# Performance work log

Measured on AMD Instinct MI355X. Metric: run time of the kernel, lower is better.

## Reference

```python
import jax, jax.numpy as jnp
import numpy as np
from jax import lax

N_G, E_G, E_LG = 100000, 400000, 1200000
N_T, E_T, E_LGT = 50000, 100000, 300000
D_F, D_MSG_G = 64, 128
VOCAB, D_EMB, D_MSG_T = 780, 128, 128
N_ITERS_G, N_ITERS_T = 4, 4
SCALE = 0.05  # keep relu/sum chains numerically tame over iterations


def setup_inputs() -> dict:
    key = jax.random.key(0)
    ks = jax.random.split(key, 32)
    f32 = jnp.float32
    w = lambda k, sh: jax.random.normal(k, sh, f32) * SCALE
    return {
        "G_f": jax.random.normal(ks[0], (N_G, D_F), f32),
        "G_ef": jax.random.normal(ks[1], (E_G, D_F), f32),
        "G_src": jax.random.randint(ks[2], (E_G,), 0, N_G, jnp.int32),
        "G_dst": jax.random.randint(ks[3], (E_G,), 0, N_G, jnp.int32),
        "G_lg_src": jax.random.randint(ks[4], (E_LG,), 0, E_G, jnp.int32),
        "G_lg_dst": jax.random.randint(ks[5], (E_LG,), 0, E_G, jnp.int32),
        "T_id": jax.random.randint(ks[6], (N_T,), 0, VOCAB, jnp.int32),
        "T_src": jax.random.randint(ks[7], (E_T,), 0, N_T, jnp.int32),
        "T_dst": jax.random.randint(ks[8], (E_T,), 0, N_T, jnp.int32),
        "T_lg_src": jax.random.randint(ks[9], (E_LGT,), 0, E_T, jnp.int32),
        "T_lg_dst": jax.random.randint(ks[10], (E_LGT,), 0, E_T, jnp.int32),
        "embeddings": jax.random.normal(ks[11], (VOCAB, D_EMB), f32),
        "W1": w(ks[12], (D_F, D_MSG_G)),
        "W2": w(ks[13], (D_F, D_MSG_G)),
        "W3": w(ks[14], (D_MSG_G, D_MSG_G)),
        "U1_G": w(ks[15], (D_F, D_MSG_G)),
        "U2_G": w(ks[16], (D_MSG_G, D_MSG_G)),
        "Wz": w(ks[17], (D_EMB, D_MSG_T)),
        "Uz": w(ks[18], (D_MSG_T, D_MSG_T)),
        "Wr": w(ks[19], (D_EMB, D_MSG_T)),
        "Ur": w(ks[20], (D_MSG_T, D_MSG_T)),
        "Wh": w(ks[21], (D_EMB, D_MSG_T)),
        "Uh": w(ks[22], (D_MSG_T, D_MSG_T)),
        "U1_T": w(ks[23], (D_EMB, D_MSG_T)),
        "U2_T": w(ks[24], (D_MSG_T, D_MSG_T)),
    }


def reference(G_f, G_ef, G_src, G_dst, G_lg_src, G_lg_dst,
              T_id, T_src, T_dst, T_lg_src, T_lg_dst,
              embeddings, W1, W2, W3, U1_G, U2_G,
              Wz, Uz, Wr, Ur, Wh, Uh, U1_T, U2_T):
    seg = jax.ops.segment_sum

    # ---- molecule graph G: loopy-BP MLP messages on the line graph ----
    f_src_G = G_f[G_src]                               # [E_G, D_F] copy_src
    base_G = f_src_G @ W1 + G_ef @ W2                  # loop-invariant part of g1_G

    def stepG(msg, _):
        sum_msg = seg(msg[G_lg_src], G_lg_dst, num_segments=E_G)
        return jax.nn.relu(base_G + sum_msg @ W3), None

    msgG0 = jnp.zeros((E_G, D_MSG_G), G_f.dtype)
    msgG, _ = lax.scan(stepG, msgG0, None, length=N_ITERS_G)

    # readout g2_G: sum edge msgs into dst nodes
    sG = seg(msgG, G_dst, num_segments=N_G)
    x_G = jax.nn.relu(G_f @ U1_G + sG @ U2_G)          # [N_G, D_MSG_G]

    # ---- junction tree T: GRU messages on the tree line graph ----
    f_T = embeddings[T_id]                             # one-hot id @ embeddings
    f_src_T = f_T[T_src]                               # [E_T, D_EMB]
    xz, xr, xh = f_src_T @ Wz, f_src_T @ Wr, f_src_T @ Wh

    def stepT(msg, _):
        s = seg(msg[T_lg_src], T_lg_dst, num_segments=E_T)
        z = jax.nn.sigmoid(xz + s @ Uz)
        r = jax.nn.sigmoid(xr + s @ Ur)
        h = jnp.tanh(xh + (r * s) @ Uh)
        return (1.0 - z) * s + z * h, None

    msgT0 = jnp.zeros((E_T, D_MSG_T), f_T.dtype)
    msgT, _ = lax.scan(stepT, msgT0, None, length=N_ITERS_T)

    sT = seg(msgT, T_dst, num_segments=N_T)
    x_T = jax.nn.relu(f_T @ U1_T + sT @ U2_T)          # [N_T, D_MSG_T]

    # concat node readouts (same width) so output is a single array
    return jnp.concatenate([x_G, x_T], axis=0)         # [N_G+N_T, 128]
```

## Files before the change

### kernel.cpp

```cpp
#include <hip/hip_runtime.h>

#define NG 100000
#define EG 400000
#define ELG 1200000
#define NT 50000
#define ET 100000
#define ELGT 300000

#define GEG ((EG + 63) / 64)
#define GET ((ET + 63) / 64)
#define GNG ((NG + 63) / 64)
#define GNT ((NT + 63) / 64)

#define SEG1 EG
#define SEG2 (EG + NG)
#define SEG3 (EG + NG + ET)
#define NSEG_ALL (EG + NG + ET + NT)
#define NE_ALL (ELG + EG + ELGT + ET)
#define NE_PAD (NE_ALL + 3 * NSEG_ALL + 64)

typedef unsigned short u16;
typedef unsigned int u32;
typedef __attribute__((ext_vector_type(8))) short bf16x8;
typedef __attribute__((ext_vector_type(4))) float f32x4;

#define TILE_B 16384

__device__ __forceinline__ float bflo(u32 p){ return __uint_as_float(p << 16); }
__device__ __forceinline__ float bfhi(u32 p){ return __uint_as_float(p & 0xffff0000u); }
__device__ __forceinline__ float bf2f(u16 h){ return __uint_as_float(((u32)h) << 16); }
__device__ __forceinline__ u16 f2bf(float f){
  u32 u = __float_as_uint(f);
  u32 r = u + 0x7fffu + ((u >> 16) & 1u);
  return (u16)(r >> 16);
}
__device__ __forceinline__ float sigm(float x){ return 1.0f / (1.0f + __expf(-x)); }
__device__ __forceinline__ float tanh_(float x){ return 2.0f / (1.0f + __expf(-2.0f * x)) - 1.0f; }
__device__ __forceinline__ float relu_(float x){ return x > 0.0f ? x : 0.0f; }
__device__ __forceinline__ void wfence(){ __builtin_amdgcn_wave_barrier(); }

__device__ __forceinline__ int swz(int r, int c){ return r * 256 + (c ^ ((r & 7) << 4)); }

__device__ __forceinline__ void zero8(float v[8]){
  #pragma unroll
  for (int j = 0; j < 8; j++) v[j] = 0.f;
}
__device__ __forceinline__ uint4 pack8(const float v[8]){
  uint4 o;
  o.x = f2bf(v[0]) | ((u32)f2bf(v[1]) << 16);
  o.y = f2bf(v[2]) | ((u32)f2bf(v[3]) << 16);
  o.z = f2bf(v[4]) | ((u32)f2bf(v[5]) << 16);
  o.w = f2bf(v[6]) | ((u32)f2bf(v[7]) << 16);
  return o;
}
__device__ __forceinline__ uint2 pack4(const f32x4& a){
  uint2 o;
  o.x = (u32)f2bf(a[0]) | ((u32)f2bf(a[1]) << 16);
  o.y = (u32)f2bf(a[2]) | ((u32)f2bf(a[3]) << 16);
  return o;
}
__device__ __forceinline__ void unp4(uint2 u, float v[4]){
  v[0] = bflo(u.x); v[1] = bfhi(u.x); v[2] = bflo(u.y); v[3] = bfhi(u.y);
}
__device__ __forceinline__ bf16x8 packfrag(const float v[8]){
  union { uint4 u; bf16x8 b; } c; c.u = pack8(v); return c.b;
}
__device__ __forceinline__ bf16x8 zfrag(){
  union { uint4 u; bf16x8 b; } c; c.u = make_uint4(0, 0, 0, 0); return c.b;
}
__device__ __forceinline__ bf16x8 as_frag(uint4 u){
  union { uint4 u; bf16x8 b; } c; c.u = u; return c.b;
}

__global__ void k_sniff(const u32* __restrict__ g, int* __restrict__ flag){
  __shared__ int sh[2];
  if (threadIdx.x < 2) sh[threadIdx.x] = 0;
  __syncthreads();
  int c0 = 0, c1 = 0;
  for (int i = 0; i < 16; i++){
    u32 w = g[threadIdx.x * 16 + i];
    u32 lo = w & 0xFFFFu;
    if (lo == 0u) c0++;
    else { u32 e = (lo >> 7) & 0xFFu; if (e >= 96u && e <= 144u) c1++; }
  }
  atomicAdd(&sh[0], c0); atomicAdd(&sh[1], c1);
  __syncthreads();
  if (threadIdx.x == 0) *flag = (sh[0] < 512 && sh[1] > 2048) ? 1 : 0;
}

__global__ void k_cvt_all(const void* p0, const void* p1, const void* p2, const void* p3,
                          const void* p4, const void* p5, const void* p6, const void* p7,
                          const void* p8, const void* p9, const void* p10, const void* p11,
                          const void* p12, float* __restrict__ wm, const int* __restrict__ flagp){
  int i = blockIdx.x * 256 + threadIdx.x;
  if (i >= 188416) return;
  const int offs[14] = {0,8192,16384,32768,40960,57344,73728,90112,106496,122880,139264,155648,172032,188416};
  const void* ps[13] = {p0,p1,p2,p3,p4,p5,p6,p7,p8,p9,p10,p11,p12};
  int w = 0;
  while (i >= offs[w + 1]) w++;
  int li = i - offs[w];
  wm[i] = (*flagp) ? bf2f(((const u16*)ps[w])[li]) : ((const float*)ps[w])[li];
}

__global__ void k_mkfrag_all(const float* __restrict__ wm, u16* __restrict__ frag){
  const int wmo[13] = {0,8192,16384,32768,40960,57344,73728,90112,106496,122880,139264,155648,172032};
  const int nks[13] = {2,2,4,2,4,4,4,4,4,4,4,4,4};
  int b = blockIdx.x;
  int wi = 0, ks = b;
  while (ks >= nks[wi]){ ks -= nks[wi]; wi++; }
  const float* W = wm + wmo[wi];
  int nt = threadIdx.x >> 6, lane = threadIdx.x & 63;
  int kr = ks * 32 + ((lane >> 4) << 3);
  int col = nt * 16 + (lane & 15);
  u16* o = frag + (size_t)b * 4096 + nt * 512 + lane * 8;
  #pragma unroll
  for (int j = 0; j < 8; j++) o[j] = f2bf(W[(size_t)(kr + j) * 128 + col]);
}

__device__ __forceinline__ const void* rowdt(const void* mat, size_t row, int W, int bf){
  return bf ? (const void*)((const u16*)mat + row * (size_t)W)
            : (const void*)((const float*)mat + row * (size_t)W);
}
__device__ __forceinline__ void load8(const void* rowbase, int c8, int bf, float v[8]){
  if (bf){
    uint4 d = ((const uint4*)rowbase)[c8];
    v[0]=bflo(d.x); v[1]=bfhi(d.x); v[2]=bflo(d.y); v[3]=bfhi(d.y);
    v[4]=bflo(d.z); v[5]=bfhi(d.z); v[6]=bflo(d.w); v[7]=bfhi(d.w);
  } else {
    const float4* p = (const float4*)rowbase + (c8 << 1);
    float4 a = p[0], b = p[1];
    v[0]=a.x; v[1]=a.y; v[2]=a.z; v[3]=a.w; v[4]=b.x; v[5]=b.y; v[6]=b.z; v[7]=b.w;
  }
}

__global__ void k_hist_all(const int* __restrict__ Glgd, const int* __restrict__ Gd,
                           const int* __restrict__ Tlgd, const int* __restrict__ Td,
                           int* __restrict__ cnt){
  int e = blockIdx.x * 256 + threadIdx.x;
  if (e >= NE_ALL) return;
  int seg;
  if (e < ELG)                       seg = Glgd[e];
  else if (e < ELG + EG)             seg = SEG1 + Gd[e - ELG];
  else if (e < ELG + EG + ELGT)      seg = SEG2 + Tlgd[e - ELG - EG];
  else                               seg = SEG3 + Td[e - ELG - EG - ELGT];
  atomicAdd(&cnt[seg], 1);
}

__global__ void k_scan1(const int* __restrict__ cnt, int n, int* __restrict__ csum){
  int base = blockIdx.x * 4096, tid = threadIdx.x;
  int s = 0;
  for (int i = 0; i < 16; i++){
    int idx = base + i * 256 + tid;
    if (idx < n) s += (cnt[idx] + 3) & ~3;
  }
  __shared__ int red[4];
  for (int off = 32; off; off >>= 1) s += __shfl_down(s, off, 64);
  if ((tid & 63) == 0) red[tid >> 6] = s;
  __syncthreads();
  if (tid == 0) csum[blockIdx.x] = red[0] + red[1] + red[2] + red[3];
}

__global__ void k_scan2(int* csum, int nch, int* rowptr, int n){
  if (threadIdx.x == 0){
    int run = 0;
    for (int c = 0; c < nch; c++){ int t = csum[c]; csum[c] = run; run += t; }
    rowptr[n] = run;
  }
}

__global__ void k_scan3(const int* __restrict__ cnt, int n, const int* __restrict__ csum,
                        int* __restrict__ rowptr){
  __shared__ int buf[4096];
  __shared__ int tsum[256];
  int base = blockIdx.x * 4096, tid = threadIdx.x;
  for (int i = 0; i < 16; i++){
    int idx = base + i * 256 + tid;
    buf[i * 256 + tid] = (idx < n) ? ((cnt[idx] + 3) & ~3) : 0;
  }
  __syncthreads();
  int run = 0;
  for (int i = 0; i < 16; i++){ int v = buf[tid * 16 + i]; buf[tid * 16 + i] = run; run += v; }
  tsum[tid] = run;
  __syncthreads();
  for (int off = 1; off < 256; off <<= 1){
    int v = (tid >= off) ? tsum[tid - off] : 0;
    __syncthreads();
    tsum[tid] += v;
    __syncthreads();
  }
  int texcl = tsum[tid] - run;
  int cbase = csum[blockIdx.x];
  for (int i = 0; i < 16; i++){
    int idx = base + tid * 16 + i;
    if (idx < n) rowptr[idx] = cbase + texcl + buf[tid * 16 + i];
  }
}

__global__ void k_fill_all(const int* __restrict__ Glgd, const int* __restrict__ Glgs,
                           const int* __restrict__ Gd,
                           const int* __restrict__ Tlgd, const int* __restrict__ Tlgs,
                           const int* __restrict__ Td,
                           const int* __restrict__ rowptr, int* __restrict__ fill,
                           int* __restrict__ col){
  int e = blockIdx.x * 256 + threadIdx.x;
  if (e >= NE_ALL) return;
  int seg, srcv;
  if (e < ELG){                      seg = Glgd[e];                           srcv = Glgs[e]; }
  else if (e < ELG + EG){            int l = e - ELG;                         seg = SEG1 + Gd[l];   srcv = l; }
  else if (e < ELG + EG + ELGT){     int l = e - ELG - EG;                    seg = SEG2 + Tlgd[l]; srcv = Tlgs[l]; }
  else {                             int l = e - ELG - EG - ELGT;             seg = SEG3 + Td[l];   srcv = l; }
  int pos = atomicAdd(&fill[seg], 1);
  col[rowptr[seg] + pos] = srcv;
}

__global__ void k_fill_pad(const int* __restrict__ cnt, const int* __restrict__ rowptr,
                           int* __restrict__ col){
  int seg = blockIdx.x * 256 + threadIdx.x;
  if (seg >= NSEG_ALL) return;
  int dummy = (seg < SEG2) ? EG : ET;
  int start = rowptr[seg] + cnt[seg];
  int end = rowptr[seg + 1];
  for (int q = start; q < end; q++) col[q] = dummy;
}

__global__ void k_zero_dummy(u16* a, u16* b, u16* c, u16* d){
  int i = threadIdx.x;
  if (i < 128){
    a[(size_t)EG * 128 + i] = 0; b[(size_t)EG * 128 + i] = 0;
    c[(size_t)ET * 128 + i] = 0; d[(size_t)ET * 128 + i] = 0;
  }
}


__device__ __forceinline__ void acc8_add(float (&a)[8], uint4 d){
  a[0] += bflo(d.x); a[1] += bfhi(d.x);
  a[2] += bflo(d.y); a[3] += bfhi(d.y);
  a[4] += bflo(d.z); a[5] += bfhi(d.z);
  a[6] += bflo(d.w); a[7] += bfhi(d.w);
}

__device__ __forceinline__ void gather_accum(const int* __restrict__ rowptr,
    const int* __restrict__ colidx, const u16* __restrict__ msg,
    int row, int M, int kg, float (&acc)[4][8])
{
  #pragma unroll
  for (int ks = 0; ks < 4; ks++) zero8(acc[ks]);
  if (row >= M) return;
  int p = rowptr[row], pe = rowptr[row + 1];
  for (; p < pe; p += 4){
    int i0 = colidx[p], i1 = colidx[p + 1], i2 = colidx[p + 2], i3 = colidx[p + 3];
    const uint4* b0 = (const uint4*)(msg + (size_t)i0 * 128);
    const uint4* b1 = (const uint4*)(msg + (size_t)i1 * 128);
    const uint4* b2 = (const uint4*)(msg + (size_t)i2 * 128);
    const uint4* b3 = (const uint4*)(msg + (size_t)i3 * 128);
    uint4 v0[4], v1[4], v2[4], v3[4];
    #pragma unroll
    for (int ks = 0; ks < 4; ks++){
      v0[ks] = b0[ks * 4 + kg]; v1[ks] = b1[ks * 4 + kg];
      v2[ks] = b2[ks * 4 + kg]; v3[ks] = b3[ks * 4 + kg];
    }
    #pragma unroll
    for (int ks = 0; ks < 4; ks++){
      acc8_add(acc[ks], v0[ks]); acc8_add(acc[ks], v1[ks]);
      acc8_add(acc[ks], v2[ks]); acc8_add(acc[ks], v3[ks]);
    }
  }
}

template<int KS>
__device__ __forceinline__ void mma_f(const bf16x8* a, const u16* __restrict__ frag,
                                      f32x4 (&acc)[8])
{
  int lane = threadIdx.x & 63;
  #pragma unroll
  for (int ks = 0; ks < KS; ks++){
    const u16* fb = frag + (size_t)ks * 4096 + lane * 8;
    #pragma unroll
    for (int nt = 0; nt < 8; nt++){
      bf16x8 b = *(const bf16x8*)(fb + (size_t)nt * 512);
      acc[nt] = __builtin_amdgcn_mfma_f32_16x16x32_bf16(a[ks], b, acc[nt], 0, 0, 0);
    }
  }
}

#define INIT_ACC(A) { _Pragma("unroll") for (int n_=0;n_<8;n_++){ A[n_][0]=0.f; A[n_][1]=0.f; A[n_][2]=0.f; A[n_][3]=0.f; } }

__device__ __forceinline__ void repack_store(const char* __restrict__ tile,
    u16* __restrict__ dst, int row0, int M)
{
  int rl = threadIdx.x >> 2, q = threadIdx.x & 3;
  int grow = row0 + rl;
  if (grow < M){
    #pragma unroll
    for (int v = 0; v < 4; v++){
      uint4 d = *(const uint4*)(tile + swz(rl, (v * 4 + q) * 16));
      *(uint4*)(dst + (size_t)grow * 128 + (size_t)(v * 4 + q) * 8) = d;
    }
  }
}

__device__ __forceinline__ size_t fslot(int blk, int w, int nt){
  return ((((size_t)blk * 4 + w) * 8 + nt) * 64 + (threadIdx.x & 63)) * 4;
}

__device__ __forceinline__ void load_catfrag(const void* __restrict__ Gf,
    const void* __restrict__ Gef, const int* __restrict__ Gsrc,
    int arow, int kg, int bf, bf16x8 (&fC)[4])
{
  if (arow < EG){
    int sr = Gsrc[arow];
    const void* ra = rowdt(Gf, (size_t)sr, 64, bf);
    const void* rb = rowdt(Gef, (size_t)arow, 64, bf);
    float t[8];
    load8(ra, kg, bf, t);     fC[0] = packfrag(t);
    load8(ra, 4 + kg, bf, t); fC[1] = packfrag(t);
    load8(rb, kg, bf, t);     fC[2] = packfrag(t);
    load8(rb, 4 + kg, bf, t); fC[3] = packfrag(t);
  } else {
    #pragma unroll
    for (int ks = 0; ks < 4; ks++) fC[ks] = zfrag();
  }
}


__global__ __launch_bounds__(256, 4) void k_init(
    const void* __restrict__ Gf, const void* __restrict__ Gef, const int* __restrict__ Gsrc,
    const u16* __restrict__ fWcat, const int* __restrict__ flagp, u16* __restrict__ msgG,
    const void* __restrict__ emb, const int* __restrict__ Tid, const int* __restrict__ Tsrc,
    const u16* __restrict__ fWz, const u16* __restrict__ fWr, const u16* __restrict__ fWh,
    u16* __restrict__ xzf, u16* __restrict__ xrf, u16* __restrict__ xhf, u16* __restrict__ msgT)
{
  __shared__ char t0[TILE_B];
  int bf = *flagp;
  int lane = threadIdx.x & 63, w = threadIdx.x >> 6;
  int stripe = w * 16, kg = lane >> 4, m16 = lane & 15;
  if (blockIdx.x < GET){
    int blk = blockIdx.x, row0 = blk * 64, arow = row0 + stripe + m16;
    bf16x8 fE[4];
    if (arow < ET){
      int id = Tid[Tsrc[arow]];
      const void* rb = rowdt(emb, (size_t)id, 128, bf);
      #pragma unroll
      for (int ks = 0; ks < 4; ks++){
        float t[8]; load8(rb, ks * 4 + kg, bf, t); fE[ks] = packfrag(t);
      }
    } else {
      #pragma unroll
      for (int ks = 0; ks < 4; ks++) fE[ks] = zfrag();
    }
    f32x4 acc[8];
    uint2 zpk[8];
    INIT_ACC(acc);
    mma_f<4>(fE, fWz, acc);
    #pragma unroll
    for (int nt = 0; nt < 8; nt++){
      zpk[nt] = pack4(acc[nt]);
      *(uint2*)(xzf + fslot(blk, w, nt)) = zpk[nt];
    }
    INIT_ACC(acc);
    mma_f<4>(fE, fWr, acc);
    #pragma unroll
    for (int nt = 0; nt < 8; nt++)
      *(uint2*)(xrf + fslot(blk, w, nt)) = pack4(acc[nt]);
    INIT_ACC(acc);
    mma_f<4>(fE, fWh, acc);
    #pragma unroll
    for (int nt = 0; nt < 8; nt++){
      *(uint2*)(xhf + fslot(blk, w, nt)) = pack4(acc[nt]);
      float xzv[4]; unp4(zpk[nt], xzv);
      #pragma unroll
      for (int r = 0; r < 4; r++){
        int rt = stripe + (kg << 2) + r;
        int cb = nt * 32 + m16 * 2;
        *(u16*)(t0 + swz(rt, cb)) = f2bf(sigm(xzv[r]) * tanh_(acc[nt][r]));
      }
    }
    wfence();
    repack_store(t0, msgT, row0, ET);
  } else {
    int blk = blockIdx.x - GET, row0 = blk * 64, arow = row0 + stripe + m16;
    bf16x8 fC[4];
    load_catfrag(Gf, Gef, Gsrc, arow, kg, bf, fC);
    f32x4 acc[8]; INIT_ACC(acc);
    mma_f<4>(fC, fWcat, acc);
    #pragma unroll
    for (int nt = 0; nt < 8; nt++)
      #pragma unroll
      for (int r = 0; r < 4; r++){
        int rt = stripe + (kg << 2) + r;
        int cb = nt * 32 + m16 * 2;
        *(u16*)(t0 + swz(rt, cb)) = f2bf(relu_(acc[nt][r]));
      }
    wfence();
    repack_store(t0, msgG, row0, EG);
  }
}

__global__ __launch_bounds__(256, 4) void k_iter(
    const u16* __restrict__ msgInG, u16* __restrict__ msgOutG,
    const void* __restrict__ Gf, const void* __restrict__ Gef, const int* __restrict__ Gsrc,
    const int* __restrict__ rp, const int* __restrict__ col,
    const u16* __restrict__ fWcat, const u16* __restrict__ fW3, const int* __restrict__ flagp,
    const u16* __restrict__ msgInT, u16* __restrict__ msgOutT,
    const u16* __restrict__ fUz, const u16* __restrict__ fUr, const u16* __restrict__ fUh,
    const u16* __restrict__ xzf, const u16* __restrict__ xrf, const u16* __restrict__ xhf)
{
  __shared__ char t0[TILE_B];
  __shared__ char t1[TILE_B];
  int lane = threadIdx.x & 63, w = threadIdx.x >> 6;
  int stripe = w * 16, kg = lane >> 4, m16 = lane & 15;
  if (blockIdx.x < GET){
    int blk = blockIdx.x, row0 = blk * 64, arow = row0 + stripe + m16;
    float ga[4][8];
    gather_accum(rp + SEG2, col, msgInT, arow, ET, kg, ga);
    bf16x8 fS[4];
    #pragma unroll
    for (int ks = 0; ks < 4; ks++){
      uint4 pk = pack8(ga[ks]);
      *(uint4*)(t0 + swz(stripe + m16, ks * 64 + kg * 16)) = pk;
      fS[ks] = as_frag(pk);
    }
    f32x4 acc[8];
    INIT_ACC(acc);
    mma_f<4>(fS, fUr, acc);
    wfence();
    #pragma unroll
    for (int nt = 0; nt < 8; nt++){
      uint2 r4 = *(const uint2*)(xrf + fslot(blk, w, nt));
      float xrv[4]; unp4(r4, xrv);
      #pragma unroll
      for (int r = 0; r < 4; r++){
        int rt = stripe + (kg << 2) + r;
        int cb = nt * 32 + m16 * 2;
        float s = bf2f(*(const u16*)(t0 + swz(rt, cb)));
        float rr = sigm(xrv[r] + acc[nt][r]);
        *(u16*)(t1 + swz(rt, cb)) = f2bf(rr * s);
      }
    }
    wfence();
    bf16x8 fRS[4];
    #pragma unroll
    for (int ks = 0; ks < 4; ks++)
      fRS[ks] = *(const bf16x8*)(t1 + swz(stripe + m16, ks * 64 + kg * 16));
    INIT_ACC(acc);
    mma_f<4>(fRS, fUh, acc);
    wfence();
    #pragma unroll
    for (int nt = 0; nt < 8; nt++){
      uint2 h4 = *(const uint2*)(xhf + fslot(blk, w, nt));
      float xhv[4]; unp4(h4, xhv);
      #pragma unroll
      for (int r = 0; r < 4; r++){
        int rt = stripe + (kg << 2) + r;
        int cb = nt * 32 + m16 * 2;
        *(u16*)(t1 + swz(rt, cb)) = f2bf(tanh_(xhv[r] + acc[nt][r]));
      }
    }
    wfence();
    bf16x8 fS2[4];
    #pragma unroll
    for (int ks = 0; ks < 4; ks++)
      fS2[ks] = *(const bf16x8*)(t0 + swz(stripe + m16, ks * 64 + kg * 16));
    INIT_ACC(acc);
    mma_f<4>(fS2, fUz, acc);
    wfence();
    #pragma unroll
    for (int nt = 0; nt < 8; nt++){
      uint2 z4 = *(const uint2*)(xzf + fslot(blk, w, nt));
      float xzv[4]; unp4(z4, xzv);
      #pragma unroll
      for (int r = 0; r < 4; r++){
        int rt = stripe + (kg << 2) + r;
        int cb = nt * 32 + m16 * 2;
        float z = sigm(xzv[r] + acc[nt][r]);
        float s = bf2f(*(const u16*)(t0 + swz(rt, cb)));
        float h = bf2f(*(const u16*)(t1 + swz(rt, cb)));
        *(u16*)(t0 + swz(rt, cb)) = f2bf((1.f - z) * s + z * h);
      }
    }
    wfence();
    repack_store(t0, msgOutT, row0, ET);
  } else {
    int bf = *flagp;
    int blk = blockIdx.x - GET, row0 = blk * 64, arow = row0 + stripe + m16;
    float ga[4][8];
    gather_accum(rp, col, msgInG, arow, EG, kg, ga);
    bf16x8 fS[4];
    #pragma unroll
    for (int ks = 0; ks < 4; ks++) fS[ks] = packfrag(ga[ks]);
    bf16x8 fC[4];
    load_catfrag(Gf, Gef, Gsrc, arow, kg, bf, fC);
    f32x4 acc[8]; INIT_ACC(acc);
    mma_f<4>(fS, fW3, acc);
    mma_f<4>(fC, fWcat, acc);
    #pragma unroll
    for (int nt = 0; nt < 8; nt++)
      #pragma unroll
      for (int r = 0; r < 4; r++){
        int rt = stripe + (kg << 2) + r;
        int cb = nt * 32 + m16 * 2;
        *(u16*)(t0 + swz(rt, cb)) = f2bf(relu_(acc[nt][r]));
      }
    wfence();
    repack_store(t0, msgOutG, row0, EG);
  }
}

__global__ __launch_bounds__(256, 4) void k_readout(
    const void* __restrict__ Gf, const u16* __restrict__ msgG,
    const int* __restrict__ rp, const int* __restrict__ col,
    const u16* __restrict__ fU1G, const u16* __restrict__ fU2G,
    const void* __restrict__ emb, const int* __restrict__ Tid, const u16* __restrict__ msgT,
    const u16* __restrict__ fU1T, const u16* __restrict__ fU2T,
    const int* __restrict__ flagp, float* __restrict__ out)
{
  int bf = *flagp;
  int lane = threadIdx.x & 63, w = threadIdx.x >> 6;
  int stripe = w * 16, kg = lane >> 4, m16 = lane & 15;
  if (blockIdx.x < GNT){
    int row0 = blockIdx.x * 64, arow = row0 + stripe + m16;
    float ga[4][8];
    gather_accum(rp + SEG3, col, msgT, arow, NT, kg, ga);
    bf16x8 fS[4];
    #pragma unroll
    for (int ks = 0; ks < 4; ks++) fS[ks] = packfrag(ga[ks]);
    bf16x8 fE[4];
    if (arow < NT){
      int id = Tid[arow];
      const void* rb = rowdt(emb, (size_t)id, 128, bf);
      #pragma unroll
      for (int ks = 0; ks < 4; ks++){
        float t[8]; load8(rb, ks * 4 + kg, bf, t); fE[ks] = packfrag(t);
      }
    } else {
      #pragma unroll
      for (int ks = 0; ks < 4; ks++) fE[ks] = zfrag();
    }
    f32x4 acc[8]; INIT_ACC(acc);
    mma_f<4>(fS, fU2T, acc);
    mma_f<4>(fE, fU1T, acc);
    #pragma unroll
    for (int nt = 0; nt < 8; nt++)
      #pragma unroll
      for (int r = 0; r < 4; r++){
        int R = row0 + stripe + (kg << 2) + r;
        if (R < NT) out[(size_t)(NG + R) * 128 + nt * 16 + m16] = relu_(acc[nt][r]);
      }
  } else {
    int row0 = (blockIdx.x - GNT) * 64, arow = row0 + stripe + m16;
    float ga[4][8];
    gather_accum(rp + SEG1, col, msgG, arow, NG, kg, ga);
    bf16x8 fS[4];
    #pragma unroll
    for (int ks = 0; ks < 4; ks++) fS[ks] = packfrag(ga[ks]);
    bf16x8 fG[2];
    if (arow < NG){
      const void* ra = rowdt(Gf, (size_t)arow, 64, bf);
      float t[8];
      load8(ra, kg, bf, t);     fG[0] = packfrag(t);
      load8(ra, 4 + kg, bf, t); fG[1] = packfrag(t);
    } else { fG[0] = zfrag(); fG[1] = zfrag(); }
    f32x4 acc[8]; INIT_ACC(acc);
    mma_f<4>(fS, fU2G, acc);
    mma_f<2>(fG, fU1G, acc);
    #pragma unroll
    for (int nt = 0; nt < 8; nt++)
      #pragma unroll
      for (int r = 0; r < 4; r++){
        int R = row0 + stripe + (kg << 2) + r;
        if (R < NG) out[(size_t)R * 128 + nt * 16 + m16] = relu_(acc[nt][r]);
      }
  }
}

extern "C" void kernel_launch(void* const* d_in, const int* in_sizes, int n_in,
                              void* d_out, int out_size, void* d_ws, size_t ws_size,
                              hipStream_t stream)
{
  const void* G_f      = d_in[0];
  const void* G_ef     = d_in[1];
  const int*  G_src    = (const int*)d_in[2];
  const int*  G_dst    = (const int*)d_in[3];
  const int*  G_lg_src = (const int*)d_in[4];
  const int*  G_lg_dst = (const int*)d_in[5];
  const int*  T_id     = (const int*)d_in[6];
  const int*  T_src    = (const int*)d_in[7];
  const int*  T_dst    = (const int*)d_in[8];
  const int*  T_lg_src = (const int*)d_in[9];
  const int*  T_lg_dst = (const int*)d_in[10];
  const void* emb      = d_in[11];
  float* out = (float*)d_out;
  (void)in_sizes; (void)n_in; (void)out_size; (void)ws_size;

  size_t off = 0;
  auto alloc = [&](size_t bytes) -> char* {
    char* p = (char*)d_ws + off;
    off += (bytes + 255) & ~(size_t)255;
    return p;
  };

  int*   flag = (int*)alloc(256);
  float* wm   = (float*)alloc(sizeof(float) * 188416);
  u16*   frag = (u16*)alloc(2 * 46 * 4096);
  const u16* fWcat = frag;
  const u16* fW3   = frag + (size_t)4  * 4096;
  const u16* fU1G  = frag + (size_t)8  * 4096;
  const u16* fU2G  = frag + (size_t)10 * 4096;
  const u16* fWz   = frag + (size_t)14 * 4096;
  const u16* fUz   = frag + (size_t)18 * 4096;
  const u16* fWr   = frag + (size_t)22 * 4096;
  const u16* fUr   = frag + (size_t)26 * 4096;
  const u16* fWh   = frag + (size_t)30 * 4096;
  const u16* fUh   = frag + (size_t)34 * 4096;
  const u16* fU1T  = frag + (size_t)38 * 4096;
  const u16* fU2T  = frag + (size_t)42 * 4096;

  int* rp   = (int*)alloc(sizeof(int) * (NSEG_ALL + 1));
  int* col  = (int*)alloc(sizeof(int) * NE_PAD);
  int* cnt  = (int*)alloc(sizeof(int) * 2 * NSEG_ALL);
  int* csum = (int*)alloc(sizeof(int) * 256);
  u16* msgGA = (u16*)alloc((size_t)(EG + 1) * 128 * 2);
  u16* msgGB = (u16*)alloc((size_t)(EG + 1) * 128 * 2);
  u16* xzf   = (u16*)alloc((size_t)GET * 8192 * 2);
  u16* xrf   = (u16*)alloc((size_t)GET * 8192 * 2);
  u16* xhf   = (u16*)alloc((size_t)GET * 8192 * 2);
  u16* msgTA = (u16*)alloc((size_t)(ET + 1) * 128 * 2);
  u16* msgTB = (u16*)alloc((size_t)(ET + 1) * 128 * 2);

  k_sniff<<<1, 256, 0, stream>>>((const u32*)G_ef, flag);
  k_cvt_all<<<(188416 + 255) / 256, 256, 0, stream>>>(
      d_in[12], d_in[13], d_in[14], d_in[15], d_in[16], d_in[17], d_in[18],
      d_in[19], d_in[20], d_in[21], d_in[22], d_in[23], d_in[24], wm, flag);
  k_mkfrag_all<<<46, 512, 0, stream>>>(wm, frag);
  k_zero_dummy<<<1, 128, 0, stream>>>(msgGA, msgGB, msgTA, msgTB);

  hipMemsetAsync(cnt, 0, sizeof(int) * 2 * NSEG_ALL, stream);
  k_hist_all<<<(NE_ALL + 255) / 256, 256, 0, stream>>>(G_lg_dst, G_dst, T_lg_dst, T_dst, cnt);
  int nch = (NSEG_ALL + 4095) / 4096;
  k_scan1<<<nch, 256, 0, stream>>>(cnt, NSEG_ALL, csum);
  k_scan2<<<1, 64, 0, stream>>>(csum, nch, rp, NSEG_ALL);
  k_scan3<<<nch, 256, 0, stream>>>(cnt, NSEG_ALL, csum, rp);
  k_fill_all<<<(NE_ALL + 255) / 256, 256, 0, stream>>>(
      G_lg_dst, G_lg_src, G_dst, T_lg_dst, T_lg_src, T_dst, rp, cnt + NSEG_ALL, col);
  k_fill_pad<<<(NSEG_ALL + 255) / 256, 256, 0, stream>>>(cnt, rp, col);

  k_init<<<GET + GEG, 256, 0, stream>>>(G_f, G_ef, G_src, fWcat, flag, msgGA,
                                        emb, T_id, T_src, fWz, fWr, fWh, xzf, xrf, xhf, msgTA);
  k_iter<<<GET + GEG, 256, 0, stream>>>(msgGA, msgGB, G_f, G_ef, G_src, rp, col, fWcat, fW3, flag,
                                        msgTA, msgTB, fUz, fUr, fUh, xzf, xrf, xhf);
  k_iter<<<GET + GEG, 256, 0, stream>>>(msgGB, msgGA, G_f, G_ef, G_src, rp, col, fWcat, fW3, flag,
                                        msgTB, msgTA, fUz, fUr, fUh, xzf, xrf, xhf);
  k_iter<<<GET + GEG, 256, 0, stream>>>(msgGA, msgGB, G_f, G_ef, G_src, rp, col, fWcat, fW3, flag,
                                        msgTA, msgTB, fUz, fUr, fUh, xzf, xrf, xhf);
  k_readout<<<GNT + GNG, 256, 0, stream>>>(G_f, msgGB, rp, col, fU1G, fU2G,
                                           emb, T_id, msgTB, fU1T, fU2T, flag, out);
}
```

Measured before the change: 1.098 ms.

## Vectorize CSR index loads, interleave T/G blocks, prefetch gate inputs, raise occupancy

Pads CSR segments to multiples of 8 so each group of four column indices can be read with a single uint4 load in the gather loop. Interleaves the smaller tree-graph blocks among the molecule-graph blocks (1 in 5 for init/iter, 1 in 3 for readout) to balance heterogeneous work across CUs. Hoists the xr/xh/xz gate-input loads ahead of the MFMA calls so their latency overlaps the matrix work. Raises launch bounds from 4 to 5 blocks per CU and uses nontemporal stores for the final output. Extra padding adds some zero-row gather work, and the higher occupancy target may force register spills.

Measured after the change: 1.661 ms. +51.3%, slower.

```diff
diff --git a/kernel.cpp b/kernel.cpp
--- a/kernel.cpp
+++ b/kernel.cpp
@@ -17,7 +17,7 @@
 #define SEG3 (EG + NG + ET)
 #define NSEG_ALL (EG + NG + ET + NT)
 #define NE_ALL (ELG + EG + ELGT + ET)
-#define NE_PAD (NE_ALL + 3 * NSEG_ALL + 64)
+#define NE_PAD (NE_ALL + 7 * NSEG_ALL + 64)
 
 typedef unsigned short u16;
 typedef unsigned int u32;
@@ -70,6 +70,23 @@
 }
 __device__ __forceinline__ bf16x8 as_frag(uint4 u){
   union { uint4 u; bf16x8 b; } c; c.u = u; return c.b;
+}
+
+__device__ __forceinline__ bool mapTG5(int bid, int& idx){
+  int q = bid / 5, r = bid - q * 5;
+  if (r == 2 && q < GET){ idx = q; return true; }
+  int before = 0;
+  if (bid >= 2){ before = (bid - 2) / 5 + 1; if (before > GET) before = GET; }
+  idx = bid - before;
+  return false;
+}
+__device__ __forceinline__ bool mapTG3(int bid, int& idx){
+  int q = bid / 3, r = bid - q * 3;
+  if (r == 1 && q < GNT){ idx = q; return true; }
+  int before = 0;
+  if (bid >= 1){ before = (bid - 1) / 3 + 1; if (before > GNT) before = GNT; }
+  idx = bid - before;
+  return false;
 }
 
 __global__ void k_sniff(const u32* __restrict__ g, int* __restrict__ flag){
@@ -151,7 +168,7 @@
   int s = 0;
   for (int i = 0; i < 16; i++){
     int idx = base + i * 256 + tid;
-    if (idx < n) s += (cnt[idx] + 3) & ~3;
+    if (idx < n) s += (cnt[idx] + 7) & ~7;
   }
   __shared__ int red[4];
   for (int off = 32; off; off >>= 1) s += __shfl_down(s, off, 64);
@@ -175,7 +192,7 @@
   int base = blockIdx.x * 4096, tid = threadIdx.x;
   for (int i = 0; i < 16; i++){
     int idx = base + i * 256 + tid;
-    buf[i * 256 + tid] = (idx < n) ? ((cnt[idx] + 3) & ~3) : 0;
+    buf[i * 256 + tid] = (idx < n) ? ((cnt[idx] + 7) & ~7) : 0;
   }
   __syncthreads();
   int run = 0;
@@ -248,11 +265,11 @@
   if (row >= M) return;
   int p = rowptr[row], pe = rowptr[row + 1];
   for (; p < pe; p += 4){
-    int i0 = colidx[p], i1 = colidx[p + 1], i2 = colidx[p + 2], i3 = colidx[p + 3];
-    const uint4* b0 = (const uint4*)(msg + (size_t)i0 * 128);
-    const uint4* b1 = (const uint4*)(msg + (size_t)i1 * 128);
-    const uint4* b2 = (const uint4*)(msg + (size_t)i2 * 128);
-    const uint4* b3 = (const uint4*)(msg + (size_t)i3 * 128);
+    uint4 ci = *(const uint4*)(colidx + p);
+    const uint4* b0 = (const uint4*)(msg + (size_t)ci.x * 128);
+    const uint4* b1 = (const uint4*)(msg + (size_t)ci.y * 128);
+    const uint4* b2 = (const uint4*)(msg + (size_t)ci.z * 128);
+    const uint4* b3 = (const uint4*)(msg + (size_t)ci.w * 128);
     uint4 v0[4], v1[4], v2[4], v3[4];
     #pragma unroll
     for (int ks = 0; ks < 4; ks++){
@@ -323,7 +340,7 @@
 }
 
 
-__global__ __launch_bounds__(256, 4) void k_init(
+__global__ __launch_bounds__(256, 5) void k_init(
     const void* __restrict__ Gf, const void* __restrict__ Gef, const int* __restrict__ Gsrc,
     const u16* __restrict__ fWcat, const int* __restrict__ flagp, u16* __restrict__ msgG,
     const void* __restrict__ emb, const int* __restrict__ Tid, const int* __restrict__ Tsrc,
@@ -334,8 +351,9 @@
   int bf = *flagp;
   int lane = threadIdx.x & 63, w = threadIdx.x >> 6;
   int stripe = w * 16, kg = lane >> 4, m16 = lane & 15;
-  if (blockIdx.x < GET){
-    int blk = blockIdx.x, row0 = blk * 64, arow = row0 + stripe + m16;
+  int idx;
+  if (mapTG5(blockIdx.x, idx)){
+    int blk = idx, row0 = blk * 64, arow = row0 + stripe + m16;
     bf16x8 fE[4];
     if (arow < ET){
       int id = Tid[Tsrc[arow]];
@@ -378,7 +396,7 @@
     wfence();
     repack_store(t0, msgT, row0, ET);
   } else {
-    int blk = blockIdx.x - GET, row0 = blk * 64, arow = row0 + stripe + m16;
+    int blk = idx, row0 = blk * 64, arow = row0 + stripe + m16;
     bf16x8 fC[4];
     load_catfrag(Gf, Gef, Gsrc, arow, kg, bf, fC);
     f32x4 acc[8]; INIT_ACC(acc);
@@ -396,7 +414,7 @@
   }
 }
 
-__global__ __launch_bounds__(256, 4) void k_iter(
+__global__ __launch_bounds__(256, 5) void k_iter(
     const u16* __restrict__ msgInG, u16* __restrict__ msgOutG,
     const void* __restrict__ Gf, const void* __restrict__ Gef, const int* __restrict__ Gsrc,
     const int* __restrict__ rp, const int* __restrict__ col,
@@ -409,8 +427,9 @@
   __shared__ char t1[TILE_B];
   int lane = threadIdx.x & 63, w = threadIdx.x >> 6;
   int stripe = w * 16, kg = lane >> 4, m16 = lane & 15;
-  if (blockIdx.x < GET){
-    int blk = blockIdx.x, row0 = blk * 64, arow = row0 + stripe + m16;
+  int idx;
+  if (mapTG5(blockIdx.x, idx)){
+    int blk = idx, row0 = blk * 64, arow = row0 + stripe + m16;
     float ga[4][8];
     gather_accum(rp + SEG2, col, msgInT, arow, ET, kg, ga);
     bf16x8 fS[4];
@@ -420,14 +439,16 @@
       *(uint4*)(t0 + swz(stripe + m16, ks * 64 + kg * 16)) = pk;
       fS[ks] = as_frag(pk);
     }
+    uint2 xr4[8];
+    #pragma unroll
+    for (int nt = 0; nt < 8; nt++) xr4[nt] = *(const uint2*)(xrf + fslot(blk, w, nt));
     f32x4 acc[8];
     INIT_ACC(acc);
     mma_f<4>(fS, fUr, acc);
     wfence();
     #pragma unroll
     for (int nt = 0; nt < 8; nt++){
-      uint2 r4 = *(const uint2*)(xrf + fslot(blk, w, nt));
-      float xrv[4]; unp4(r4, xrv);
+      float xrv[4]; unp4(xr4[nt], xrv);
       #pragma unroll
       for (int r = 0; r < 4; r++){
         int rt = stripe + (kg << 2) + r;
@@ -442,13 +463,15 @@
     #pragma unroll
     for (int ks = 0; ks < 4; ks++)
       fRS[ks] = *(const bf16x8*)(t1 + swz(stripe + m16, ks * 64 + kg * 16));
+    uint2 xh4[8];
+    #pragma unroll
+    for (int nt = 0; nt < 8; nt++) xh4[nt] = *(const uint2*)(xhf + fslot(blk, w, nt));
     INIT_ACC(acc);
     mma_f<4>(fRS, fUh, acc);
     wfence();
     #pragma unroll
     for (int nt = 0; nt < 8; nt++){
-      uint2 h4 = *(const uint2*)(xhf + fslot(blk, w, nt));
-      float xhv[4]; unp4(h4, xhv);
+      float xhv[4]; unp4(xh4[nt], xhv);
       #pragma unroll
       for (int r = 0; r < 4; r++){
         int rt = stripe + (kg << 2) + r;
@@ -461,13 +484,15 @@
     #pragma unroll
     for (int ks = 0; ks < 4; ks++)
       fS2[ks] = *(const bf16x8*)(t0 + swz(stripe + m16, ks * 64 + kg * 16));
+    uint2 xz4[8];
+    #pragma unroll
+    for (int nt = 0; nt < 8; nt++) xz4[nt] = *(const uint2*)(xzf + fslot(blk, w, nt));
     INIT_ACC(acc);
     mma_f<4>(fS2, fUz, acc);
     wfence();
     #pragma unroll
     for (int nt = 0; nt < 8; nt++){
-      uint2 z4 = *(const uint2*)(xzf + fslot(blk, w, nt));
-      float xzv[4]; unp4(z4, xzv);
+      float xzv[4]; unp4(xz4[nt], xzv);
       #pragma unroll
       for (int r = 0; r < 4; r++){
         int rt = stripe + (kg << 2) + r;
@@ -482,7 +507,7 @@
     repack_store(t0, msgOutT, row0, ET);
   } else {
     int bf = *flagp;
-    int blk = blockIdx.x - GET, row0 = blk * 64, arow = row0 + stripe + m16;
+    int blk = idx, row0 = blk * 64, arow = row0 + stripe + m16;
     float ga[4][8];
     gather_accum(rp, col, msgInG, arow, EG, kg, ga);
     bf16x8 fS[4];
@@ -506,7 +531,7 @@
   }
 }
 
-__global__ __launch_bounds__(256, 4) void k_readout(
+__global__ __launch_bounds__(256, 5) void k_readout(
     const void* __restrict__ Gf, const u16* __restrict__ msgG,
     const int* __restrict__ rp, const int* __restrict__ col,
     const u16* __restrict__ fU1G, const u16* __restrict__ fU2G,
@@ -517,8 +542,9 @@
   int bf = *flagp;
   int lane = threadIdx.x & 63, w = threadIdx.x >> 6;
   int stripe = w * 16, kg = lane >> 4, m16 = lane & 15;
-  if (blockIdx.x < GNT){
-    int row0 = blockIdx.x * 64, arow = row0 + stripe + m16;
+  int idx;
+  if (mapTG3(blockIdx.x, idx)){
+    int row0 = idx * 64, arow = row0 + stripe + m16;
     float ga[4][8];
     gather_accum(rp + SEG3, col, msgT, arow, NT, kg, ga);
     bf16x8 fS[4];
@@ -544,10 +570,11 @@
       #pragma unroll
       for (int r = 0; r < 4; r++){
         int R = row0 + stripe + (kg << 2) + r;
-        if (R < NT) out[(size_t)(NG + R) * 128 + nt * 16 + m16] = relu_(acc[nt][r]);
+        if (R < NT) __builtin_nontemporal_store(relu_(acc[nt][r]),
+                        &out[(size_t)(NG + R) * 128 + nt * 16 + m16]);
       }
   } else {
-    int row0 = (blockIdx.x - GNT) * 64, arow = row0 + stripe + m16;
+    int row0 = idx * 64, arow = row0 + stripe + m16;
     float ga[4][8];
     gather_accum(rp + SEG1, col, msgG, arow, NG, kg, ga);
     bf16x8 fS[4];
@@ -568,7 +595,8 @@
       #pragma unroll
       for (int r = 0; r < 4; r++){
         int R = row0 + stripe + (kg << 2) + r;
-        if (R < NG) out[(size_t)R * 128 + nt * 16 + m16] = relu_(acc[nt][r]);
+        if (R < NG) __builtin_nontemporal_store(relu_(acc[nt][r]),
+                        &out[(size_t)R * 128 + nt * 16 + m16]);
       }
   }
 }
```
